# Performance work log

Measured on AMD Instinct MI355X. Metric: run time of the kernel, lower is better.

The kernel has to match this reference:

```python
import jax, jax.numpy as jnp
import numpy as np

EMBED_DIM = 1536
BOTTLENECK = 64
EPS = 1e-5  # torch LayerNorm default


def setup_inputs() -> dict:
    key = jax.random.key(0)
    ks = jax.random.split(key, 6)
    x = jax.random.normal(ks[0], (32768, EMBED_DIM), dtype=jnp.float32)
    # Xavier-uniform init for down (matches nn.init.xavier_uniform_)
    limit = float(np.sqrt(6.0 / (EMBED_DIM + BOTTLENECK)))
    w_down = jax.random.uniform(ks[1], (BOTTLENECK, EMBED_DIM), jnp.float32, -limit, limit)
    b_down = jnp.zeros((BOTTLENECK,), jnp.float32)
    # Torch initializes up to zeros; use small random values so gradients/outputs are non-trivial
    w_up = jax.random.normal(ks[2], (EMBED_DIM, BOTTLENECK), dtype=jnp.float32) * 0.02
    b_up = jnp.zeros((EMBED_DIM,), jnp.float32)
    gamma = jnp.ones((EMBED_DIM,), jnp.float32)
    beta = jnp.zeros((EMBED_DIM,), jnp.float32)
    return {"x": x, "w_down": w_down, "b_down": b_down, "w_up": w_up,
            "b_up": b_up, "gamma": gamma, "beta": beta}


def reference(x, w_down, b_down, w_up, b_up, gamma, beta):
    residual = x
    # LayerNorm over last dim
    mean = jnp.mean(x, axis=-1, keepdims=True)
    var = jnp.mean(jnp.square(x - mean), axis=-1, keepdims=True)
    h = (x - mean) * jax.lax.rsqrt(var + EPS) * gamma + beta
    # down-proj -> exact GELU -> (dropout=identity at inference) -> up-proj
    h = jnp.einsum('nd,bd->nb', h, w_down) + b_down  # [N, 64]
    h = jax.nn.gelu(h, approximate=False)            # torch F.gelu default (erf)
    h = jnp.einsum('nb,db->nd', h, w_up) + b_up      # [N, 1536]
    out = residual + h
    # F.normalize(p=2, dim=-1) with eps=1e-12
    norm = jnp.maximum(jnp.linalg.norm(out, axis=-1, keepdims=True), 1e-12)
    return out / norm
```

## Files before the change

kernel.cpp:

```cpp
#include <hip/hip_runtime.h>
#include <math.h>

#define EMBED 1536
#define BN 64
#define XS_STRIDE 1544
#define GS_STRIDE 80

typedef __attribute__((ext_vector_type(8))) short short8;
typedef __attribute__((ext_vector_type(4))) float f32x4;

__device__ inline unsigned short f2bf(float f) {
    union { float f; unsigned u; } c; c.f = f;
    unsigned u = c.u;
    return (unsigned short)((u + 0x7fffu + ((u >> 16) & 1u)) >> 16);
}
__device__ inline float bf2f(unsigned short h) {
    union { unsigned u; float f; } c; c.u = ((unsigned)h) << 16;
    return c.f;
}

__global__ void prep_kernel(const float* __restrict__ w_down, const float* __restrict__ w_up,
                            const float* __restrict__ gamma, const float* __restrict__ beta,
                            unsigned short* __restrict__ wdg, unsigned short* __restrict__ wub,
                            float* __restrict__ c1, float* __restrict__ c2) {
    int blk = blockIdx.x;
    if (blk < 384) {
        int i = blk * 256 + threadIdx.x;
        int d = i % EMBED;
        wdg[i] = f2bf(w_down[i] * gamma[d]);
        wub[i] = f2bf(w_up[i]);
        return;
    }
    int b = blk - 384;
    int t = threadIdx.x;
    float s1 = 0.f, s2 = 0.f;
    for (int d = t; d < EMBED; d += 256) {
        float w = w_down[b * EMBED + d];
        s1 += gamma[d] * w;
        s2 += beta[d] * w;
    }
    #pragma unroll
    for (int m = 1; m < 64; m <<= 1) { s1 += __shfl_xor(s1, m); s2 += __shfl_xor(s2, m); }
    __shared__ float r1[4], r2[4];
    int wave = t >> 6, lane = t & 63;
    if (lane == 0) { r1[wave] = s1; r2[wave] = s2; }
    __syncthreads();
    if (t == 0) {
        c1[b] = r1[0] + r1[1] + r1[2] + r1[3];
        c2[b] = r2[0] + r2[1] + r2[2] + r2[3];
    }
}

__global__ __launch_bounds__(256, 3) void fused_kernel(
    const float* __restrict__ x, const float* __restrict__ b_down,
    const float* __restrict__ b_up,
    const unsigned short* __restrict__ wdg, const unsigned short* __restrict__ wub,
    const float* __restrict__ c1, const float* __restrict__ c2,
    float* __restrict__ out)
{
    __shared__ unsigned short xs[16 * XS_STRIDE];
    __shared__ unsigned short gs[16 * GS_STRIDE];
    __shared__ float mean_s[16], rstd_s[16], sumsq_s[16], inv_s[16];

    const int tid  = threadIdx.x;
    const int wave = tid >> 6, lane = tid & 63;
    const int l16  = lane & 15, quad = lane >> 4;
    const long row0 = (long)blockIdx.x * 16;

    {
        float4 v[4][6];
        #pragma unroll
        for (int j = 0; j < 4; ++j) {
            const float4* xp = (const float4*)(x + (row0 + wave * 4 + j) * EMBED);
            #pragma unroll
            for (int k = 0; k < 6; ++k) v[j][k] = xp[lane + 64 * k];
        }
        #pragma unroll
        for (int j = 0; j < 4; ++j) {
            int lr = wave * 4 + j;
            float s = 0.f, ss = 0.f;
            #pragma unroll
            for (int k = 0; k < 6; ++k) {
                s  += v[j][k].x + v[j][k].y + v[j][k].z + v[j][k].w;
                ss += v[j][k].x * v[j][k].x + v[j][k].y * v[j][k].y
                    + v[j][k].z * v[j][k].z + v[j][k].w * v[j][k].w;
            }
            #pragma unroll
            for (int m = 1; m < 64; m <<= 1) { s += __shfl_xor(s, m); ss += __shfl_xor(ss, m); }
            float mean = s * (1.f / EMBED);
            float var  = ss * (1.f / EMBED) - mean * mean;
            if (lane == 0) {
                mean_s[lr] = mean;
                rstd_s[lr] = rsqrtf(var + 1e-5f);
                sumsq_s[lr] = 0.f;
            }
            #pragma unroll
            for (int k = 0; k < 6; ++k) {
                ushort4 p;
                p.x = f2bf(v[j][k].x); p.y = f2bf(v[j][k].y);
                p.z = f2bf(v[j][k].z); p.w = f2bf(v[j][k].w);
                *(ushort4*)(&xs[lr * XS_STRIDE + 4 * (lane + 64 * k)]) = p;
            }
        }
    }
    __syncthreads();

    f32x4 acc = {0.f, 0.f, 0.f, 0.f};
    {
        const unsigned short* arow = &xs[l16 * XS_STRIDE];
        const unsigned short* brow = wdg + (size_t)(wave * 16 + l16) * EMBED;
        #pragma unroll 4
        for (int kk = 0; kk < 48; ++kk) {
            int ko = kk * 32 + quad * 8;
            short8 a = *(const short8*)(arow + ko);
            short8 b = *(const short8*)(brow + ko);
            acc = __builtin_amdgcn_mfma_f32_16x16x32_bf16(a, b, acc, 0, 0, 0);
        }
    }
    {
        int bg = wave * 16 + l16;
        float c1v = c1[bg], c2v = c2[bg], bdv = b_down[bg];
        #pragma unroll
        for (int reg = 0; reg < 4; ++reg) {
            int r = quad * 4 + reg;
            float rs = rstd_s[r];
            float v = rs * acc[reg] - rs * mean_s[r] * c1v + c2v + bdv;
            float g = 0.5f * v * (1.f + erff(v * 0.70710678118654752f));
            gs[r * GS_STRIDE + bg] = f2bf(g);
        }
    }
    __syncthreads();

    short8 gb0 = *(const short8*)(&gs[l16 * GS_STRIDE + quad * 8]);
    short8 gb1 = *(const short8*)(&gs[l16 * GS_STRIDE + 32 + quad * 8]);
    const int dbase = wave * 384;
    f32x4 cc[24];
    float sqs = 0.f;
    #pragma unroll
    for (int t = 0; t < 24; ++t) {
        int d0 = dbase + t * 16;
        int dm = d0 + quad * 4;
        float4 bu = *(const float4*)(b_up + dm);
        ushort4 rx = *(const ushort4*)(&xs[l16 * XS_STRIDE + dm]);
        f32x4 c;
        c[0] = bf2f(rx.x) + bu.x;
        c[1] = bf2f(rx.y) + bu.y;
        c[2] = bf2f(rx.z) + bu.z;
        c[3] = bf2f(rx.w) + bu.w;
        const unsigned short* wrow = wub + (size_t)(d0 + l16) * 64;
        short8 a0 = *(const short8*)(wrow + quad * 8);
        short8 a1 = *(const short8*)(wrow + 32 + quad * 8);
        c = __builtin_amdgcn_mfma_f32_16x16x32_bf16(a0, gb0, c, 0, 0, 0);
        c = __builtin_amdgcn_mfma_f32_16x16x32_bf16(a1, gb1, c, 0, 0, 0);
        cc[t] = c;
        sqs += c[0] * c[0] + c[1] * c[1] + c[2] * c[2] + c[3] * c[3];
    }
    sqs += __shfl_xor(sqs, 16);
    sqs += __shfl_xor(sqs, 32);
    if (lane < 16) atomicAdd(&sumsq_s[l16], sqs);
    __syncthreads();
    if (tid < 16) inv_s[tid] = 1.f / fmaxf(sqrtf(sumsq_s[tid]), 1e-12f);
    __syncthreads();

    const float inv = inv_s[l16];
    float* orow = out + (row0 + l16) * EMBED;
    #pragma unroll
    for (int t = 0; t < 24; ++t) {
        int dm = dbase + t * 16 + quad * 4;
        f32x4 c = cc[t];
        float4 o;
        o.x = c[0] * inv; o.y = c[1] * inv; o.z = c[2] * inv; o.w = c[3] * inv;
        *(float4*)(orow + dm) = o;
    }
}

extern "C" void kernel_launch(void* const* d_in, const int* in_sizes, int n_in,
                              void* d_out, int out_size, void* d_ws, size_t ws_size,
                              hipStream_t stream)
{
    const float* x      = (const float*)d_in[0];
    const float* w_down = (const float*)d_in[1];
    const float* b_down = (const float*)d_in[2];
    const float* w_up   = (const float*)d_in[3];
    const float* b_up   = (const float*)d_in[4];
    const float* gamma  = (const float*)d_in[5];
    const float* beta   = (const float*)d_in[6];
    float* out = (float*)d_out;

    const int N = in_sizes[0] / EMBED;

    unsigned short* wdg = (unsigned short*)d_ws;
    unsigned short* wub = wdg + BN * EMBED;
    float* c1 = (float*)(wub + BN * EMBED);
    float* c2 = c1 + BN;

    prep_kernel<<<384 + BN, 256, 0, stream>>>(w_down, w_up, gamma, beta, wdg, wub, c1, c2);
    fused_kernel<<<N / 16, 256, 0, stream>>>(x, b_down, b_up, wdg, wub, c1, c2, out);
}
```

Measured before the change: 421.7 us.

## Use 512-thread blocks and recompute up-projection instead of holding results in registers

The fused kernel now runs 8 waves per 16-row block. Only the first 4 waves do the down-projection, and each wave covers half as many output columns in the up-projection. The 24 per-thread accumulator tiles are no longer kept live across the norm reduction. The up-projection MFMAs and bias/residual adds are computed again in the output pass after the row norm is known. This frees registers for higher occupancy, at the cost of doubled up-projection work and extra weight and LDS reads.

```diff
diff --git a/kernel.cpp b/kernel.cpp
--- a/kernel.cpp
+++ b/kernel.cpp
@@ -51,7 +51,7 @@
     }
 }
 
-__global__ __launch_bounds__(256, 3) void fused_kernel(
+__global__ __launch_bounds__(512, 6) void fused_kernel(
     const float* __restrict__ x, const float* __restrict__ b_down,
     const float* __restrict__ b_up,
     const unsigned short* __restrict__ wdg, const unsigned short* __restrict__ wub,
@@ -60,7 +60,7 @@
 {
     __shared__ unsigned short xs[16 * XS_STRIDE];
     __shared__ unsigned short gs[16 * GS_STRIDE];
-    __shared__ float mean_s[16], rstd_s[16], sumsq_s[16], inv_s[16];
+    __shared__ float mean_s[16], rstd_s[16], sumsq_s[16];
 
     const int tid  = threadIdx.x;
     const int wave = tid >> 6, lane = tid & 63;
@@ -68,16 +68,16 @@
     const long row0 = (long)blockIdx.x * 16;
 
     {
-        float4 v[4][6];
+        float4 v[2][6];
         #pragma unroll
-        for (int j = 0; j < 4; ++j) {
-            const float4* xp = (const float4*)(x + (row0 + wave * 4 + j) * EMBED);
+        for (int j = 0; j < 2; ++j) {
+            const float4* xp = (const float4*)(x + (row0 + wave * 2 + j) * EMBED);
             #pragma unroll
             for (int k = 0; k < 6; ++k) v[j][k] = xp[lane + 64 * k];
         }
         #pragma unroll
-        for (int j = 0; j < 4; ++j) {
-            int lr = wave * 4 + j;
+        for (int j = 0; j < 2; ++j) {
+            int lr = wave * 2 + j;
             float s = 0.f, ss = 0.f;
             #pragma unroll
             for (int k = 0; k < 6; ++k) {
@@ -105,39 +105,40 @@
     }
     __syncthreads();
 
-    f32x4 acc = {0.f, 0.f, 0.f, 0.f};
-    {
-        const unsigned short* arow = &xs[l16 * XS_STRIDE];
-        const unsigned short* brow = wdg + (size_t)(wave * 16 + l16) * EMBED;
-        #pragma unroll 4
-        for (int kk = 0; kk < 48; ++kk) {
-            int ko = kk * 32 + quad * 8;
-            short8 a = *(const short8*)(arow + ko);
-            short8 b = *(const short8*)(brow + ko);
-            acc = __builtin_amdgcn_mfma_f32_16x16x32_bf16(a, b, acc, 0, 0, 0);
-        }
-    }
-    {
-        int bg = wave * 16 + l16;
-        float c1v = c1[bg], c2v = c2[bg], bdv = b_down[bg];
-        #pragma unroll
-        for (int reg = 0; reg < 4; ++reg) {
-            int r = quad * 4 + reg;
-            float rs = rstd_s[r];
-            float v = rs * acc[reg] - rs * mean_s[r] * c1v + c2v + bdv;
-            float g = 0.5f * v * (1.f + erff(v * 0.70710678118654752f));
-            gs[r * GS_STRIDE + bg] = f2bf(g);
+    if (wave < 4) {
+        f32x4 acc = {0.f, 0.f, 0.f, 0.f};
+        {
+            const unsigned short* arow = &xs[l16 * XS_STRIDE];
+            const unsigned short* brow = wdg + (size_t)(wave * 16 + l16) * EMBED;
+            #pragma unroll 4
+            for (int kk = 0; kk < 48; ++kk) {
+                int ko = kk * 32 + quad * 8;
+                short8 a = *(const short8*)(arow + ko);
+                short8 b = *(const short8*)(brow + ko);
+                acc = __builtin_amdgcn_mfma_f32_16x16x32_bf16(a, b, acc, 0, 0, 0);
+            }
+        }
+        {
+            int bg = wave * 16 + l16;
+            float c1v = c1[bg], c2v = c2[bg], bdv = b_down[bg];
+            #pragma unroll
+            for (int reg = 0; reg < 4; ++reg) {
+                int r = quad * 4 + reg;
+                float rs = rstd_s[r];
+                float v = rs * acc[reg] - rs * mean_s[r] * c1v + c2v + bdv;
+                float g = 0.5f * v * (1.f + erff(v * 0.70710678118654752f));
+                gs[r * GS_STRIDE + bg] = f2bf(g);
+            }
         }
     }
     __syncthreads();
 
     short8 gb0 = *(const short8*)(&gs[l16 * GS_STRIDE + quad * 8]);
     short8 gb1 = *(const short8*)(&gs[l16 * GS_STRIDE + 32 + quad * 8]);
-    const int dbase = wave * 384;
-    f32x4 cc[24];
+    const int dbase = wave * 192;
     float sqs = 0.f;
-    #pragma unroll
-    for (int t = 0; t < 24; ++t) {
+    #pragma unroll 4
+    for (int t = 0; t < 12; ++t) {
         int d0 = dbase + t * 16;
         int dm = d0 + quad * 4;
         float4 bu = *(const float4*)(b_up + dm);
@@ -152,22 +153,31 @@
         short8 a1 = *(const short8*)(wrow + 32 + quad * 8);
         c = __builtin_amdgcn_mfma_f32_16x16x32_bf16(a0, gb0, c, 0, 0, 0);
         c = __builtin_amdgcn_mfma_f32_16x16x32_bf16(a1, gb1, c, 0, 0, 0);
-        cc[t] = c;
         sqs += c[0] * c[0] + c[1] * c[1] + c[2] * c[2] + c[3] * c[3];
     }
     sqs += __shfl_xor(sqs, 16);
     sqs += __shfl_xor(sqs, 32);
     if (lane < 16) atomicAdd(&sumsq_s[l16], sqs);
     __syncthreads();
-    if (tid < 16) inv_s[tid] = 1.f / fmaxf(sqrtf(sumsq_s[tid]), 1e-12f);
-    __syncthreads();
-
-    const float inv = inv_s[l16];
+
+    const float inv = 1.f / fmaxf(sqrtf(sumsq_s[l16]), 1e-12f);
     float* orow = out + (row0 + l16) * EMBED;
-    #pragma unroll
-    for (int t = 0; t < 24; ++t) {
-        int dm = dbase + t * 16 + quad * 4;
-        f32x4 c = cc[t];
+    #pragma unroll 4
+    for (int t = 0; t < 12; ++t) {
+        int d0 = dbase + t * 16;
+        int dm = d0 + quad * 4;
+        float4 bu = *(const float4*)(b_up + dm);
+        ushort4 rx = *(const ushort4*)(&xs[l16 * XS_STRIDE + dm]);
+        f32x4 c;
+        c[0] = bf2f(rx.x) + bu.x;
+        c[1] = bf2f(rx.y) + bu.y;
+        c[2] = bf2f(rx.z) + bu.z;
+        c[3] = bf2f(rx.w) + bu.w;
+        const unsigned short* wrow = wub + (size_t)(d0 + l16) * 64;
+        short8 a0 = *(const short8*)(wrow + quad * 8);
+        short8 a1 = *(const short8*)(wrow + 32 + quad * 8);
+        c = __builtin_amdgcn_mfma_f32_16x16x32_bf16(a0, gb0, c, 0, 0, 0);
+        c = __builtin_amdgcn_mfma_f32_16x16x32_bf16(a1, gb1, c, 0, 0, 0);
         float4 o;
         o.x = c[0] * inv; o.y = c[1] * inv; o.z = c[2] * inv; o.w = c[3] * inv;
         *(float4*)(orow + dm) = o;
@@ -195,5 +205,5 @@
     float* c2 = c1 + BN;
 
     prep_kernel<<<384 + BN, 256, 0, stream>>>(w_down, w_up, gamma, beta, wdg, wub, c1, c2);
-    fused_kernel<<<N / 16, 256, 0, stream>>>(x, b_down, b_up, wdg, wub, c1, c2, out);
-}
+    fused_kernel<<<N / 16, 512, 0, stream>>>(x, b_down, b_up, wdg, wub, c1, c2, out);
+}
```

After: 455.8 us. +8.1%, slower.

## Make fused kernel persistent with atomic tile queue and prefetch next tile

Applied to the files above, without the earlier changes.

Replaces the one-block-per-tile grid with a persistent grid of 768 blocks that pull 16-row tiles from a global atomic counter, which the prep kernel resets. After staging the current tile into LDS, each block issues the global loads for the next tile into registers so they overlap with the two MFMA GEMMs and the epilogue. The point is to hide HBM load latency and cut block launch and tail overhead. In exchange, the register-held prefetch raises register pressure, which may lower occupancy below the launch-bounds target of 3 blocks per CU, and every tile now costs one atomic.

```diff
diff --git a/kernel.cpp b/kernel.cpp
--- a/kernel.cpp
+++ b/kernel.cpp
@@ -5,6 +5,7 @@
 #define BN 64
 #define XS_STRIDE 1544
 #define GS_STRIDE 80
+#define NT_GRID 768
 
 typedef __attribute__((ext_vector_type(8))) short short8;
 typedef __attribute__((ext_vector_type(4))) float f32x4;
@@ -22,8 +23,10 @@
 __global__ void prep_kernel(const float* __restrict__ w_down, const float* __restrict__ w_up,
                             const float* __restrict__ gamma, const float* __restrict__ beta,
                             unsigned short* __restrict__ wdg, unsigned short* __restrict__ wub,
-                            float* __restrict__ c1, float* __restrict__ c2) {
+                            float* __restrict__ c1, float* __restrict__ c2,
+                            int* __restrict__ cnt, int cnt_init) {
     int blk = blockIdx.x;
+    if (blk == 0 && threadIdx.x == 0) *cnt = cnt_init;
     if (blk < 384) {
         int i = blk * 256 + threadIdx.x;
         int d = i % EMBED;
@@ -56,25 +59,31 @@
     const float* __restrict__ b_up,
     const unsigned short* __restrict__ wdg, const unsigned short* __restrict__ wub,
     const float* __restrict__ c1, const float* __restrict__ c2,
-    float* __restrict__ out)
+    float* __restrict__ out, int* __restrict__ cnt, int ntiles)
 {
     __shared__ unsigned short xs[16 * XS_STRIDE];
     __shared__ unsigned short gs[16 * GS_STRIDE];
-    __shared__ float mean_s[16], rstd_s[16], sumsq_s[16], inv_s[16];
+    __shared__ float mean_s[16], rstd_s[16], sumsq_s[2][16];
+    __shared__ int tile_s;
 
     const int tid  = threadIdx.x;
     const int wave = tid >> 6, lane = tid & 63;
     const int l16  = lane & 15, quad = lane >> 4;
-    const long row0 = (long)blockIdx.x * 16;
-
+
+    int tcur = blockIdx.x;
+    float4 v[4][6];
     {
-        float4 v[4][6];
+        const long row0 = (long)tcur * 16;
         #pragma unroll
         for (int j = 0; j < 4; ++j) {
             const float4* xp = (const float4*)(x + (row0 + wave * 4 + j) * EMBED);
             #pragma unroll
             for (int k = 0; k < 6; ++k) v[j][k] = xp[lane + 64 * k];
         }
+    }
+
+    int parity = 0;
+    for (;;) {
         #pragma unroll
         for (int j = 0; j < 4; ++j) {
             int lr = wave * 4 + j;
@@ -92,7 +101,7 @@
             if (lane == 0) {
                 mean_s[lr] = mean;
                 rstd_s[lr] = rsqrtf(var + 1e-5f);
-                sumsq_s[lr] = 0.f;
+                sumsq_s[parity][lr] = 0.f;
             }
             #pragma unroll
             for (int k = 0; k < 6; ++k) {
@@ -102,75 +111,90 @@
                 *(ushort4*)(&xs[lr * XS_STRIDE + 4 * (lane + 64 * k)]) = p;
             }
         }
-    }
-    __syncthreads();
-
-    f32x4 acc = {0.f, 0.f, 0.f, 0.f};
-    {
-        const unsigned short* arow = &xs[l16 * XS_STRIDE];
-        const unsigned short* brow = wdg + (size_t)(wave * 16 + l16) * EMBED;
-        #pragma unroll 4
-        for (int kk = 0; kk < 48; ++kk) {
-            int ko = kk * 32 + quad * 8;
-            short8 a = *(const short8*)(arow + ko);
-            short8 b = *(const short8*)(brow + ko);
-            acc = __builtin_amdgcn_mfma_f32_16x16x32_bf16(a, b, acc, 0, 0, 0);
-        }
-    }
-    {
-        int bg = wave * 16 + l16;
-        float c1v = c1[bg], c2v = c2[bg], bdv = b_down[bg];
-        #pragma unroll
-        for (int reg = 0; reg < 4; ++reg) {
-            int r = quad * 4 + reg;
-            float rs = rstd_s[r];
-            float v = rs * acc[reg] - rs * mean_s[r] * c1v + c2v + bdv;
-            float g = 0.5f * v * (1.f + erff(v * 0.70710678118654752f));
-            gs[r * GS_STRIDE + bg] = f2bf(g);
-        }
-    }
-    __syncthreads();
-
-    short8 gb0 = *(const short8*)(&gs[l16 * GS_STRIDE + quad * 8]);
-    short8 gb1 = *(const short8*)(&gs[l16 * GS_STRIDE + 32 + quad * 8]);
-    const int dbase = wave * 384;
-    f32x4 cc[24];
-    float sqs = 0.f;
-    #pragma unroll
-    for (int t = 0; t < 24; ++t) {
-        int d0 = dbase + t * 16;
-        int dm = d0 + quad * 4;
-        float4 bu = *(const float4*)(b_up + dm);
-        ushort4 rx = *(const ushort4*)(&xs[l16 * XS_STRIDE + dm]);
-        f32x4 c;
-        c[0] = bf2f(rx.x) + bu.x;
-        c[1] = bf2f(rx.y) + bu.y;
-        c[2] = bf2f(rx.z) + bu.z;
-        c[3] = bf2f(rx.w) + bu.w;
-        const unsigned short* wrow = wub + (size_t)(d0 + l16) * 64;
-        short8 a0 = *(const short8*)(wrow + quad * 8);
-        short8 a1 = *(const short8*)(wrow + 32 + quad * 8);
-        c = __builtin_amdgcn_mfma_f32_16x16x32_bf16(a0, gb0, c, 0, 0, 0);
-        c = __builtin_amdgcn_mfma_f32_16x16x32_bf16(a1, gb1, c, 0, 0, 0);
-        cc[t] = c;
-        sqs += c[0] * c[0] + c[1] * c[1] + c[2] * c[2] + c[3] * c[3];
-    }
-    sqs += __shfl_xor(sqs, 16);
-    sqs += __shfl_xor(sqs, 32);
-    if (lane < 16) atomicAdd(&sumsq_s[l16], sqs);
-    __syncthreads();
-    if (tid < 16) inv_s[tid] = 1.f / fmaxf(sqrtf(sumsq_s[tid]), 1e-12f);
-    __syncthreads();
-
-    const float inv = inv_s[l16];
-    float* orow = out + (row0 + l16) * EMBED;
-    #pragma unroll
-    for (int t = 0; t < 24; ++t) {
-        int dm = dbase + t * 16 + quad * 4;
-        f32x4 c = cc[t];
-        float4 o;
-        o.x = c[0] * inv; o.y = c[1] * inv; o.z = c[2] * inv; o.w = c[3] * inv;
-        *(float4*)(orow + dm) = o;
+        if (tid == 0) tile_s = atomicAdd(cnt, 1);
+        __syncthreads();
+
+        const int tnext = tile_s;
+        const bool have_next = (tnext < ntiles);
+        if (have_next) {
+            const long row0 = (long)tnext * 16;
+            #pragma unroll
+            for (int j = 0; j < 4; ++j) {
+                const float4* xp = (const float4*)(x + (row0 + wave * 4 + j) * EMBED);
+                #pragma unroll
+                for (int k = 0; k < 6; ++k) v[j][k] = xp[lane + 64 * k];
+            }
+        }
+
+        f32x4 acc = {0.f, 0.f, 0.f, 0.f};
+        {
+            const unsigned short* arow = &xs[l16 * XS_STRIDE];
+            const unsigned short* brow = wdg + (size_t)(wave * 16 + l16) * EMBED;
+            #pragma unroll 4
+            for (int kk = 0; kk < 48; ++kk) {
+                int ko = kk * 32 + quad * 8;
+                short8 a = *(const short8*)(arow + ko);
+                short8 b = *(const short8*)(brow + ko);
+                acc = __builtin_amdgcn_mfma_f32_16x16x32_bf16(a, b, acc, 0, 0, 0);
+            }
+        }
+        {
+            int bg = wave * 16 + l16;
+            float c1v = c1[bg], c2v = c2[bg], bdv = b_down[bg];
+            #pragma unroll
+            for (int reg = 0; reg < 4; ++reg) {
+                int r = quad * 4 + reg;
+                float rs = rstd_s[r];
+                float vv = rs * acc[reg] - rs * mean_s[r] * c1v + c2v + bdv;
+                float g = 0.5f * vv * (1.f + erff(vv * 0.70710678118654752f));
+                gs[r * GS_STRIDE + bg] = f2bf(g);
+            }
+        }
+        __syncthreads();
+
+        short8 gb0 = *(const short8*)(&gs[l16 * GS_STRIDE + quad * 8]);
+        short8 gb1 = *(const short8*)(&gs[l16 * GS_STRIDE + 32 + quad * 8]);
+        const int dbase = wave * 384;
+        f32x4 cc[24];
+        float sqs = 0.f;
+        #pragma unroll
+        for (int t = 0; t < 24; ++t) {
+            int d0 = dbase + t * 16;
+            int dm = d0 + quad * 4;
+            float4 bu = *(const float4*)(b_up + dm);
+            ushort4 rx = *(const ushort4*)(&xs[l16 * XS_STRIDE + dm]);
+            f32x4 c;
+            c[0] = bf2f(rx.x) + bu.x;
+            c[1] = bf2f(rx.y) + bu.y;
+            c[2] = bf2f(rx.z) + bu.z;
+            c[3] = bf2f(rx.w) + bu.w;
+            const unsigned short* wrow = wub + (size_t)(d0 + l16) * 64;
+            short8 a0 = *(const short8*)(wrow + quad * 8);
+            short8 a1 = *(const short8*)(wrow + 32 + quad * 8);
+            c = __builtin_amdgcn_mfma_f32_16x16x32_bf16(a0, gb0, c, 0, 0, 0);
+            c = __builtin_amdgcn_mfma_f32_16x16x32_bf16(a1, gb1, c, 0, 0, 0);
+            cc[t] = c;
+            sqs += c[0] * c[0] + c[1] * c[1] + c[2] * c[2] + c[3] * c[3];
+        }
+        sqs += __shfl_xor(sqs, 16);
+        sqs += __shfl_xor(sqs, 32);
+        if (lane < 16) atomicAdd(&sumsq_s[parity][l16], sqs);
+        __syncthreads();
+
+        const float inv = 1.f / fmaxf(sqrtf(sumsq_s[parity][l16]), 1e-12f);
+        float* orow = out + ((long)tcur * 16 + l16) * EMBED;
+        #pragma unroll
+        for (int t = 0; t < 24; ++t) {
+            int dm = dbase + t * 16 + quad * 4;
+            f32x4 c = cc[t];
+            float4 o;
+            o.x = c[0] * inv; o.y = c[1] * inv; o.z = c[2] * inv; o.w = c[3] * inv;
+            *(float4*)(orow + dm) = o;
+        }
+
+        if (!have_next) break;
+        tcur = tnext;
+        parity ^= 1;
     }
 }
 
@@ -188,12 +212,16 @@
     float* out = (float*)d_out;
 
     const int N = in_sizes[0] / EMBED;
+    const int ntiles = N / 16;
+    const int grid = ntiles < NT_GRID ? ntiles : NT_GRID;
 
     unsigned short* wdg = (unsigned short*)d_ws;
     unsigned short* wub = wdg + BN * EMBED;
     float* c1 = (float*)(wub + BN * EMBED);
     float* c2 = c1 + BN;
-
-    prep_kernel<<<384 + BN, 256, 0, stream>>>(w_down, w_up, gamma, beta, wdg, wub, c1, c2);
-    fused_kernel<<<N / 16, 256, 0, stream>>>(x, b_down, b_up, wdg, wub, c1, c2, out);
-}
+    int* cnt  = (int*)(c2 + BN);
+
+    prep_kernel<<<384 + BN, 256, 0, stream>>>(w_down, w_up, gamma, beta, wdg, wub, c1, c2,
+                                              cnt, grid);
+    fused_kernel<<<grid, 256, 0, stream>>>(x, b_down, b_up, wdg, wub, c1, c2, out, cnt, ntiles);
+}
```

New measurement: 730.8 us. 1.73x slower.

## Use persistent producer/consumer warp-specialized blocks with double-buffered LDS tiles

Applied to the files above, without the earlier changes.

Replaces the one-tile-per-block launch with 256 persistent blocks of 512 threads. Four producer waves load and layer-normalize the next 16-row tile into one LDS buffer while four consumer waves run the down/up MFMA projections and write output for the previous tile from the other buffer. The goal is to overlap global x loads with compute and stores. In exchange, occupancy drops to one block per CU, only 256 blocks are launched (which may not fill all CUs), and every iteration adds block-wide barriers.

```diff
diff --git a/kernel.cpp b/kernel.cpp
--- a/kernel.cpp
+++ b/kernel.cpp
@@ -5,6 +5,7 @@
 #define BN 64
 #define XS_STRIDE 1544
 #define GS_STRIDE 80
+#define NBLOCKS 256
 
 typedef __attribute__((ext_vector_type(8))) short short8;
 typedef __attribute__((ext_vector_type(4))) float f32x4;
@@ -51,126 +52,142 @@
     }
 }
 
-__global__ __launch_bounds__(256, 3) void fused_kernel(
+__global__ __launch_bounds__(512, 1) void fused_kernel(
     const float* __restrict__ x, const float* __restrict__ b_down,
     const float* __restrict__ b_up,
     const unsigned short* __restrict__ wdg, const unsigned short* __restrict__ wub,
     const float* __restrict__ c1, const float* __restrict__ c2,
-    float* __restrict__ out)
+    float* __restrict__ out, int ntiles, int nblk)
 {
-    __shared__ unsigned short xs[16 * XS_STRIDE];
+    __shared__ unsigned short xs[2][16 * XS_STRIDE];
     __shared__ unsigned short gs[16 * GS_STRIDE];
-    __shared__ float mean_s[16], rstd_s[16], sumsq_s[16], inv_s[16];
+    __shared__ float mean_s[2][16], rstd_s[2][16], sumsq_s[2][16];
 
     const int tid  = threadIdx.x;
     const int wave = tid >> 6, lane = tid & 63;
     const int l16  = lane & 15, quad = lane >> 4;
-    const long row0 = (long)blockIdx.x * 16;
-
-    {
-        float4 v[4][6];
-        #pragma unroll
-        for (int j = 0; j < 4; ++j) {
-            const float4* xp = (const float4*)(x + (row0 + wave * 4 + j) * EMBED);
-            #pragma unroll
-            for (int k = 0; k < 6; ++k) v[j][k] = xp[lane + 64 * k];
+    const int cw   = wave - 4;
+    const int bid  = blockIdx.x;
+
+    float4 v[4][6];
+    f32x4 cc[24];
+
+    for (int it = 0; it <= nblk; ++it) {
+        const int pb = it & 1;
+        const int cb = pb ^ 1;
+        const int q  = it & 1;
+        const long tprod = (long)bid * nblk + it;
+        const long tcons = tprod - 1;
+        const bool pact = (wave < 4)  && (it < nblk) && (tprod < ntiles);
+        const bool cact = (wave >= 4) && (it > 0)    && (tcons < ntiles);
+
+        if (pact) {
+            const long row0 = tprod * 16;
+            #pragma unroll
+            for (int j = 0; j < 4; ++j) {
+                const float4* xp = (const float4*)(x + (row0 + wave * 4 + j) * EMBED);
+                #pragma unroll
+                for (int k = 0; k < 6; ++k) v[j][k] = xp[lane + 64 * k];
+            }
+        } else if (cact) {
+            f32x4 acc = {0.f, 0.f, 0.f, 0.f};
+            {
+                const unsigned short* arow = &xs[cb][l16 * XS_STRIDE];
+                const unsigned short* brow = wdg + (size_t)(cw * 16 + l16) * EMBED;
+                #pragma unroll 4
+                for (int kk = 0; kk < 48; ++kk) {
+                    int ko = kk * 32 + quad * 8;
+                    short8 a = *(const short8*)(arow + ko);
+                    short8 b = *(const short8*)(brow + ko);
+                    acc = __builtin_amdgcn_mfma_f32_16x16x32_bf16(a, b, acc, 0, 0, 0);
+                }
+            }
+            int bg = cw * 16 + l16;
+            float c1v = c1[bg], c2v = c2[bg], bdv = b_down[bg];
+            #pragma unroll
+            for (int reg = 0; reg < 4; ++reg) {
+                int r = quad * 4 + reg;
+                float rs = rstd_s[cb][r];
+                float vv = rs * acc[reg] - rs * mean_s[cb][r] * c1v + c2v + bdv;
+                float g = 0.5f * vv * (1.f + erff(vv * 0.70710678118654752f));
+                gs[r * GS_STRIDE + bg] = f2bf(g);
+            }
         }
-        #pragma unroll
-        for (int j = 0; j < 4; ++j) {
-            int lr = wave * 4 + j;
-            float s = 0.f, ss = 0.f;
-            #pragma unroll
-            for (int k = 0; k < 6; ++k) {
-                s  += v[j][k].x + v[j][k].y + v[j][k].z + v[j][k].w;
-                ss += v[j][k].x * v[j][k].x + v[j][k].y * v[j][k].y
-                    + v[j][k].z * v[j][k].z + v[j][k].w * v[j][k].w;
-            }
-            #pragma unroll
-            for (int m = 1; m < 64; m <<= 1) { s += __shfl_xor(s, m); ss += __shfl_xor(ss, m); }
-            float mean = s * (1.f / EMBED);
-            float var  = ss * (1.f / EMBED) - mean * mean;
-            if (lane == 0) {
-                mean_s[lr] = mean;
-                rstd_s[lr] = rsqrtf(var + 1e-5f);
-                sumsq_s[lr] = 0.f;
-            }
-            #pragma unroll
-            for (int k = 0; k < 6; ++k) {
-                ushort4 p;
-                p.x = f2bf(v[j][k].x); p.y = f2bf(v[j][k].y);
-                p.z = f2bf(v[j][k].z); p.w = f2bf(v[j][k].w);
-                *(ushort4*)(&xs[lr * XS_STRIDE + 4 * (lane + 64 * k)]) = p;
+        __syncthreads();
+
+        if (pact) {
+            #pragma unroll
+            for (int j = 0; j < 4; ++j) {
+                int lr = wave * 4 + j;
+                float s = 0.f, ss = 0.f;
+                #pragma unroll
+                for (int k = 0; k < 6; ++k) {
+                    s  += v[j][k].x + v[j][k].y + v[j][k].z + v[j][k].w;
+                    ss += v[j][k].x * v[j][k].x + v[j][k].y * v[j][k].y
+                        + v[j][k].z * v[j][k].z + v[j][k].w * v[j][k].w;
+                }
+                #pragma unroll
+                for (int m = 1; m < 64; m <<= 1) { s += __shfl_xor(s, m); ss += __shfl_xor(ss, m); }
+                float mean = s * (1.f / EMBED);
+                float var  = ss * (1.f / EMBED) - mean * mean;
+                if (lane == 0) {
+                    mean_s[pb][lr] = mean;
+                    rstd_s[pb][lr] = rsqrtf(var + 1e-5f);
+                }
+                #pragma unroll
+                for (int k = 0; k < 6; ++k) {
+                    ushort4 p;
+                    p.x = f2bf(v[j][k].x); p.y = f2bf(v[j][k].y);
+                    p.z = f2bf(v[j][k].z); p.w = f2bf(v[j][k].w);
+                    *(ushort4*)(&xs[pb][lr * XS_STRIDE + 4 * (lane + 64 * k)]) = p;
+                }
+            }
+        } else if (wave >= 4) {
+            if (cw == 0 && lane < 16) sumsq_s[q ^ 1][lane] = 0.f;
+            if (cact) {
+                short8 gb0 = *(const short8*)(&gs[l16 * GS_STRIDE + quad * 8]);
+                short8 gb1 = *(const short8*)(&gs[l16 * GS_STRIDE + 32 + quad * 8]);
+                const int dbase = cw * 384;
+                float sqs = 0.f;
+                #pragma unroll
+                for (int t = 0; t < 24; ++t) {
+                    int d0 = dbase + t * 16;
+                    int dm = d0 + quad * 4;
+                    float4 bu = *(const float4*)(b_up + dm);
+                    ushort4 rx = *(const ushort4*)(&xs[cb][l16 * XS_STRIDE + dm]);
+                    f32x4 c;
+                    c[0] = bf2f(rx.x) + bu.x;
+                    c[1] = bf2f(rx.y) + bu.y;
+                    c[2] = bf2f(rx.z) + bu.z;
+                    c[3] = bf2f(rx.w) + bu.w;
+                    const unsigned short* wrow = wub + (size_t)(d0 + l16) * 64;
+                    short8 a0 = *(const short8*)(wrow + quad * 8);
+                    short8 a1 = *(const short8*)(wrow + 32 + quad * 8);
+                    c = __builtin_amdgcn_mfma_f32_16x16x32_bf16(a0, gb0, c, 0, 0, 0);
+                    c = __builtin_amdgcn_mfma_f32_16x16x32_bf16(a1, gb1, c, 0, 0, 0);
+                    cc[t] = c;
+                    sqs += c[0] * c[0] + c[1] * c[1] + c[2] * c[2] + c[3] * c[3];
+                }
+                sqs += __shfl_xor(sqs, 16);
+                sqs += __shfl_xor(sqs, 32);
+                if (lane < 16) atomicAdd(&sumsq_s[q][l16], sqs);
             }
         }
-    }
-    __syncthreads();
-
-    f32x4 acc = {0.f, 0.f, 0.f, 0.f};
-    {
-        const unsigned short* arow = &xs[l16 * XS_STRIDE];
-        const unsigned short* brow = wdg + (size_t)(wave * 16 + l16) * EMBED;
-        #pragma unroll 4
-        for (int kk = 0; kk < 48; ++kk) {
-            int ko = kk * 32 + quad * 8;
-            short8 a = *(const short8*)(arow + ko);
-            short8 b = *(const short8*)(brow + ko);
-            acc = __builtin_amdgcn_mfma_f32_16x16x32_bf16(a, b, acc, 0, 0, 0);
+        __syncthreads();
+
+        if (cact) {
+            const float inv = 1.f / fmaxf(sqrtf(sumsq_s[q][l16]), 1e-12f);
+            float* orow = out + (tcons * 16 + l16) * EMBED;
+            const int dbase = cw * 384;
+            #pragma unroll
+            for (int t = 0; t < 24; ++t) {
+                int dm = dbase + t * 16 + quad * 4;
+                f32x4 c = cc[t];
+                float4 o;
+                o.x = c[0] * inv; o.y = c[1] * inv; o.z = c[2] * inv; o.w = c[3] * inv;
+                *(float4*)(orow + dm) = o;
+            }
         }
-    }
-    {
-        int bg = wave * 16 + l16;
-        float c1v = c1[bg], c2v = c2[bg], bdv = b_down[bg];
-        #pragma unroll
-        for (int reg = 0; reg < 4; ++reg) {
-            int r = quad * 4 + reg;
-            float rs = rstd_s[r];
-            float v = rs * acc[reg] - rs * mean_s[r] * c1v + c2v + bdv;
-            float g = 0.5f * v * (1.f + erff(v * 0.70710678118654752f));
-            gs[r * GS_STRIDE + bg] = f2bf(g);
-        }
-    }
-    __syncthreads();
-
-    short8 gb0 = *(const short8*)(&gs[l16 * GS_STRIDE + quad * 8]);
-    short8 gb1 = *(const short8*)(&gs[l16 * GS_STRIDE + 32 + quad * 8]);
-    const int dbase = wave * 384;
-    f32x4 cc[24];
-    float sqs = 0.f;
-    #pragma unroll
-    for (int t = 0; t < 24; ++t) {
-        int d0 = dbase + t * 16;
-        int dm = d0 + quad * 4;
-        float4 bu = *(const float4*)(b_up + dm);
-        ushort4 rx = *(const ushort4*)(&xs[l16 * XS_STRIDE + dm]);
-        f32x4 c;
-        c[0] = bf2f(rx.x) + bu.x;
-        c[1] = bf2f(rx.y) + bu.y;
-        c[2] = bf2f(rx.z) + bu.z;
-        c[3] = bf2f(rx.w) + bu.w;
-        const unsigned short* wrow = wub + (size_t)(d0 + l16) * 64;
-        short8 a0 = *(const short8*)(wrow + quad * 8);
-        short8 a1 = *(const short8*)(wrow + 32 + quad * 8);
-        c = __builtin_amdgcn_mfma_f32_16x16x32_bf16(a0, gb0, c, 0, 0, 0);
-        c = __builtin_amdgcn_mfma_f32_16x16x32_bf16(a1, gb1, c, 0, 0, 0);
-        cc[t] = c;
-        sqs += c[0] * c[0] + c[1] * c[1] + c[2] * c[2] + c[3] * c[3];
-    }
-    sqs += __shfl_xor(sqs, 16);
-    sqs += __shfl_xor(sqs, 32);
-    if (lane < 16) atomicAdd(&sumsq_s[l16], sqs);
-    __syncthreads();
-    if (tid < 16) inv_s[tid] = 1.f / fmaxf(sqrtf(sumsq_s[tid]), 1e-12f);
-    __syncthreads();
-
-    const float inv = inv_s[l16];
-    float* orow = out + (row0 + l16) * EMBED;
-    #pragma unroll
-    for (int t = 0; t < 24; ++t) {
-        int dm = dbase + t * 16 + quad * 4;
-        f32x4 c = cc[t];
-        float4 o;
-        o.x = c[0] * inv; o.y = c[1] * inv; o.z = c[2] * inv; o.w = c[3] * inv;
-        *(float4*)(orow + dm) = o;
     }
 }
 
@@ -188,6 +205,8 @@
     float* out = (float*)d_out;
 
     const int N = in_sizes[0] / EMBED;
+    const int ntiles = N / 16;
+    const int nblk = (ntiles + NBLOCKS - 1) / NBLOCKS;
 
     unsigned short* wdg = (unsigned short*)d_ws;
     unsigned short* wub = wdg + BN * EMBED;
@@ -195,5 +214,6 @@
     float* c2 = c1 + BN;
 
     prep_kernel<<<384 + BN, 256, 0, stream>>>(w_down, w_up, gamma, beta, wdg, wub, c1, c2);
-    fused_kernel<<<N / 16, 256, 0, stream>>>(x, b_down, b_up, wdg, wub, c1, c2, out);
-}
+    fused_kernel<<<NBLOCKS, 512, 0, stream>>>(x, b_down, b_up, wdg, wub, c1, c2, out,
+                                              ntiles, nblk);
+}
```

New measurement: 565.9 us. 1.34x slower.
